# Performance work log

Measured on AMD Instinct MI355X. Metric: run time of the kernel, lower is better.

The kernel has to match this reference:

```python
import jax, jax.numpy as jnp
import numpy as np

B, S, D_MODEL, N_HEADS, MAX_LEN = 2, 1024, 1024, 16, 1024
D_K = D_MODEL // N_HEADS


def setup_inputs() -> dict:
    key = jax.random.key(0)
    ks = jax.random.split(key, 8)
    w_std = 1.0 / np.sqrt(D_MODEL)  # ~ torch Linear default scale
    inp = {
        "query": jax.random.normal(ks[0], (B, S, D_MODEL), jnp.float32),
        "key": jax.random.normal(ks[1], (B, S, D_MODEL), jnp.float32),
        "value": jax.random.normal(ks[2], (B, S, D_MODEL), jnp.float32),
        "Wq": jax.random.normal(ks[3], (D_MODEL, D_MODEL), jnp.float32) * w_std,
        "Wk": jax.random.normal(ks[4], (D_MODEL, D_MODEL), jnp.float32) * w_std,
        "Wv": jax.random.normal(ks[5], (D_MODEL, D_MODEL), jnp.float32) * w_std,
        "Wo": jax.random.normal(ks[6], (D_MODEL, D_MODEL), jnp.float32) * w_std,
        "bq": jnp.zeros((D_MODEL,), jnp.float32),
        "bk": jnp.zeros((D_MODEL,), jnp.float32),
        "bv": jnp.zeros((D_MODEL,), jnp.float32),
        "bo": jnp.zeros((D_MODEL,), jnp.float32),
        "Er": jax.random.normal(ks[7], (2 * MAX_LEN - 1, D_K), jnp.float32) * 0.02,
    }
    return inp


def _rel_positions(q_len, k_len, max_len):
    pos = jnp.arange(q_len)[:, None] - jnp.arange(k_len)[None, :]
    pos = jnp.clip(pos, -max_len + 1, max_len - 1)
    return pos + max_len - 1  # [q_len, k_len] indices into Er


def reference(query, key, value, Wq, Wk, Wv, Wo, bq, bk, bv, bo, Er):
    b, q_len, d_model = query.shape
    k_len = key.shape[1]
    d_k = Er.shape[-1]
    h = d_model // d_k
    scale = 1.0 / np.sqrt(d_k)

    def proj(x, W, bias):  # torch Linear: x @ W.T + b, then split heads -> [b,h,s,d_k]
        y = x @ W.T + bias
        return y.reshape(b, -1, h, d_k).transpose(0, 2, 1, 3)

    q = proj(query, Wq, bq)
    k = proj(key, Wk, bk)
    v = proj(value, Wv, bv)

    positions = _rel_positions(q_len, k_len, MAX_LEN)  # [q,k]
    # QEr[b,h,q,k] = sum_d q[b,h,q,d] * Er[positions[q,k], d]
    # computed as a full contraction against Er then a gather on the relative axis
    qe_all = jnp.einsum('bhqd,rd->bhqr', q, Er)  # [b,h,q,2*max_len-1]
    qer = jnp.take_along_axis(qe_all, positions[None, None, :, :], axis=-1)  # [b,h,q,k]

    qk = jnp.einsum('bhqd,bhkd->bhqk', q, k)
    scores = (qk + qer) * scale
    p_attn = jax.nn.softmax(scores, axis=-1)  # dropout=0.0 (eval)
    out = jnp.einsum('bhqk,bhkd->bhqd', p_attn, v)

    out = out.transpose(0, 2, 1, 3).reshape(b, q_len, h * d_k)
    return out @ Wo.T + bo
```

## Files before the change

kernel.cpp:

```cpp
#include <hip/hip_runtime.h>
#include <hip/hip_bf16.h>
#include <cstdint>
#include <cstddef>

typedef __attribute__((ext_vector_type(8))) short bf16x8;
typedef __attribute__((ext_vector_type(4))) float f32x4;
typedef unsigned short u16;
typedef unsigned int u32;

#define DEV static __device__ __forceinline__

constexpr int Sc = 1024, DMc = 1024, Hc = 16, DKc = 64;

DEV u16 f2bf(float f) {
  u32 u = __float_as_uint(f);
  return (u16)((u + 0x7FFFu + ((u >> 16) & 1u)) >> 16);
}
DEV float bf2f(u16 h) { return __uint_as_float(((u32)h) << 16); }

DEV u32 cvtpk(float a, float b) {
  u32 r;
  asm("v_cvt_pk_bf16_f32 %0, %1, %2" : "=v"(r) : "v"(a), "v"(b));
  return r;
}

#define GLDS16(g, l)                                                        \
  __builtin_amdgcn_global_load_lds(                                         \
      (const __attribute__((address_space(1))) void*)(g),                   \
      (__attribute__((address_space(3))) void*)(l), 16, 0, 0)

struct CvtJob { const float* in; u16* out; int rsh; int nreal; };
struct CvtArgs { CvtJob j[8]; int cum[8]; };

__global__ __launch_bounds__(256) void cvt_kernel(CvtArgs a) {
  int g = (int)(blockIdx.x * 256 + threadIdx.x);
  int jb = 0, base = 0;
  #pragma unroll
  for (int k = 0; k < 7; ++k) {
    bool m = g >= a.cum[k];
    jb += m ? 1 : 0;
    base = m ? a.cum[k] : base;
  }
  CvtJob job = a.j[jb];
  int ci = g - base;
  bf16x8 o = {};
  if (ci < job.nreal) {
    const float* src = job.in + (size_t)ci * 8;
    float4 v0 = *(const float4*)src;
    float4 v1 = *(const float4*)(src + 4);
    o[0] = (short)f2bf(v0.x); o[1] = (short)f2bf(v0.y);
    o[2] = (short)f2bf(v0.z); o[3] = (short)f2bf(v0.w);
    o[4] = (short)f2bf(v1.x); o[5] = (short)f2bf(v1.y);
    o[6] = (short)f2bf(v1.z); o[7] = (short)f2bf(v1.w);
  }
  int row = ci >> job.rsh;
  int co = (ci & ~7) | ((ci & 7) ^ (row & 7));
  *(bf16x8*)(job.out + (size_t)co * 8) = o;
}

struct GemmJob { const u16* A; const u16* W; const float* bias; void* out; const float* aux; };
struct GemmArgs { GemmJob p[3]; };

template<int BM, int BN, int MODE>
__global__ __launch_bounds__(256, 2) void gemm_bt(GemmArgs G) {
  constexpr int MI = BM / 32, NI = BN / 32;
  __shared__ __align__(16) u16 sA[2][BM * 64];
  __shared__ __align__(16) u16 sB[2][BN * 64];
  const int tid = threadIdx.x, lane = tid & 63, w = tid >> 6;
  const int cl = lane & 15, rg = lane >> 4;
  const int srow = lane >> 3, schk = lane & 7;
  int z, m0, n0;
  if (MODE == 0) {
    int id = blockIdx.x;
    if (id < 512) {
      z = id >> 8;
      int r = id & 255, xcd = r & 7, t = r >> 3;
      m0 = (xcd * 4 + (t & 3)) * 64;
      n0 = (t >> 2) * 128;
    } else {
      z = 2;
      int r = id - 512, xcd = r & 7, t = r >> 3;
      n0 = (xcd * 2 + (t & 1)) * 128;
      m0 = (t >> 1) * 64;
    }
  } else {
    z = 0;
    int id = blockIdx.x, xcd = id & 7, t = id >> 3;
    m0 = (xcd * 4 + (t & 3)) * 64;
    n0 = (t >> 2) * 64;
  }
  GemmJob P = G.p[z];
  constexpr int K = 1024;
  const int wm = (w >> 1) * (BM / 2), wn = (w & 1) * (BN / 2);
  f32x4 acc[MI][NI] = {};

  bf16x8 ma[2][2];
  float  ml[2][2];

  auto stage = [&](int kt, int b) {
    if (MODE == 0) {
      const u16* Ab = P.A + (size_t)m0 * K + kt * 64;
      #pragma unroll
      for (int i = 0; i < BM / 32; ++i)
        GLDS16(Ab + (size_t)(i * 32 + w * 8 + srow) * K + schk * 8, &sA[b][(i * 32 + w * 8) * 64]);
    } else {
      #pragma unroll
      for (int i = 0; i < 2; ++i) {
        int ch = i * 256 + tid, row = ch >> 3, c = ch & 7;
        int rgl = m0 + row, bb = rgl >> 10, s = rgl & 1023;
        const u16* o0 = P.A + ((size_t)(bb * 16 + kt) * 1024 + s) * 64 + c * 8;
        ma[i][0] = *(const bf16x8*)o0;
        ma[i][1] = *(const bf16x8*)(o0 + (size_t)32 * 1024 * 64);
        ml[i][0] = P.aux[(size_t)(bb * 16 + kt) * 1024 + s];
        ml[i][1] = P.aux[(size_t)(32 + bb * 16 + kt) * 1024 + s];
      }
    }
    const u16* Wb = P.W + (size_t)n0 * K + kt * 64;
    #pragma unroll
    for (int i = 0; i < BN / 32; ++i)
      GLDS16(Wb + (size_t)(i * 32 + w * 8 + srow) * K + schk * 8, &sB[b][(i * 32 + w * 8) * 64]);
  };

  auto commit = [&](int b) {
    #pragma unroll
    for (int i = 0; i < 2; ++i) {
      int ch = i * 256 + tid, row = ch >> 3, c = ch & 7;
      float rinv = 1.0f / (ml[i][0] + ml[i][1]);
      u32 pk[4];
      #pragma unroll
      for (int p = 0; p < 4; ++p) {
        float v0 = (bf2f((u16)ma[i][0][2 * p])     + bf2f((u16)ma[i][1][2 * p]))     * rinv;
        float v1 = (bf2f((u16)ma[i][0][2 * p + 1]) + bf2f((u16)ma[i][1][2 * p + 1])) * rinv;
        pk[p] = cvtpk(v0, v1);
      }
      bf16x8 v8;
      #pragma unroll
      for (int p = 0; p < 4; ++p) {
        v8[2 * p]     = (short)(pk[p] & 0xFFFF);
        v8[2 * p + 1] = (short)(pk[p] >> 16);
      }
      *(bf16x8*)(sA[b] + row * 64 + (c ^ (row & 7)) * 8) = v8;
    }
  };

  stage(0, 0);
  if (MODE == 1) commit(0);
  for (int kt = 0; kt < 16; ++kt) {
    __syncthreads();
    const int b = kt & 1;
    if (kt < 15) stage(kt + 1, b ^ 1);
    const u16* A_ = sA[b];
    const u16* B_ = sB[b];
    #pragma unroll
    for (int kk = 0; kk < 2; ++kk) {
      bf16x8 af[MI], bfr[NI];
      #pragma unroll
      for (int mi = 0; mi < MI; ++mi) {
        int row = wm + mi * 16 + cl;
        af[mi] = *(const bf16x8*)(A_ + row * 64 + ((kk * 4 + rg) ^ (row & 7)) * 8);
      }
      #pragma unroll
      for (int ni = 0; ni < NI; ++ni) {
        int row = wn + ni * 16 + cl;
        bfr[ni] = *(const bf16x8*)(B_ + row * 64 + ((kk * 4 + rg) ^ (row & 7)) * 8);
      }
      #pragma unroll
      for (int mi = 0; mi < MI; ++mi)
        #pragma unroll
        for (int ni = 0; ni < NI; ++ni)
          acc[mi][ni] = __builtin_amdgcn_mfma_f32_16x16x32_bf16(af[mi], bfr[ni], acc[mi][ni], 0, 0, 0);
    }
    if (MODE == 1 && kt < 15) commit(b ^ 1);
  }
  #pragma unroll
  for (int mi = 0; mi < MI; ++mi) {
    #pragma unroll
    for (int ni = 0; ni < NI; ++ni) {
      #pragma unroll
      for (int j = 0; j < 4; ++j) {
        int m = m0 + wm + mi * 16 + rg * 4 + j;
        int n = n0 + wn + ni * 16 + cl;
        if (MODE == 1) {
          ((float*)P.out)[(size_t)m * DMc + n] = acc[mi][ni][j] + P.bias[n];
        } else if (z < 2) {
          float v = acc[mi][ni][j] + P.bias[n];
          int h = n >> 6, d = n & 63;
          int c2 = (d >> 3) ^ (m & 7);
          ((u16*)P.out)[((size_t)((m >> 10) * Hc + h) * Sc + (m & 1023)) * DKc + c2 * 8 + (d & 7)] = f2bf(v);
        } else {
          float v = acc[mi][ni][j] + P.bias[m];
          int d = m & 63, h = m >> 6, bb = n >> 10, s = n & 1023;
          int c2 = ((s & 63) >> 3) ^ (d & 7);
          ((u16*)P.out)[((size_t)(bb * Hc + h) * DKc + d) * Sc + (s & ~63) + c2 * 8 + (s & 7)] = f2bf(v);
        }
      }
    }
  }
}

__global__ __launch_bounds__(256, 4) void attn_rel(
    const u16* __restrict__ qg, const u16* __restrict__ kg,
    const u16* __restrict__ vtg, const u16* __restrict__ erg,
    u16* __restrict__ Opart, float* __restrict__ lpart) {
  __shared__ __align__(16) u16 sK[64 * 64];
  __shared__ __align__(16) u16 sV[64 * 64];
  __shared__ __align__(16) u16 sU[4][1440];
  const int tid = threadIdx.x, lane = tid & 63, w = tid >> 6;
  const int cl = lane & 15, rg = lane >> 4;
  const int key = cl & 7;
  const int bh = blockIdx.x & 31, qt = (blockIdx.x >> 5) & 15, half = blockIdx.x >> 9;
  const int q0 = qt * 64, t0 = half * 8;

  const u16* qrow = qg + ((size_t)bh * Sc + q0 + w * 16 + cl) * DKc;
  bf16x8 qf0 = *(const bf16x8*)(qrow + (rg ^ key) * 8);
  bf16x8 qf1 = *(const bf16x8*)(qrow + ((rg + 4) ^ key) * 8);
  f32x4 oacc[4] = {};
  float lsum = 0.f;
  u16* Uw = sU[w];
  const u16* kbase = kg + (size_t)bh * Sc * DKc;
  const u16* vbase = vtg + (size_t)bh * DKc * Sc;

  auto stage = [&](int t) {
    const u16* ks = kbase + t * 64 * 64;
    #pragma unroll
    for (int i = 0; i < 2; ++i) {
      GLDS16(ks + (i * 32 + w * 8) * 64 + lane * 8, &sK[(i * 32 + w * 8) * 64]);
      GLDS16(vbase + (size_t)(i * 32 + w * 8 + (lane >> 3)) * Sc + t * 64 + (lane & 7) * 8,
             &sV[(i * 32 + w * 8) * 64]);
    }
  };

  stage(t0);
  for (int tt = 0; tt < 8; ++tt) {
    const int t = t0 + tt;
    __syncthreads();

    f32x4 sct[4];
    __builtin_amdgcn_s_setprio(1);
    #pragma unroll
    for (int nc = 0; nc < 4; ++nc) {
      const u16* kr = sK + (nc * 16 + cl) * 64;
      bf16x8 b0 = *(const bf16x8*)(kr + (rg ^ key) * 8);
      bf16x8 b1 = *(const bf16x8*)(kr + ((rg + 4) ^ key) * 8);
      f32x4 a = {};
      a = __builtin_amdgcn_mfma_f32_16x16x32_bf16(b0, qf0, a, 0, 0, 0);
      a = __builtin_amdgcn_mfma_f32_16x16x32_bf16(b1, qf1, a, 0, 0, 0);
      sct[nc] = a;
    }
    __builtin_amdgcn_s_setprio(0);
    const u16* ebase = erg + (size_t)(q0 + w * 16 - t * 64 + 960) * DKc;
    #pragma unroll
    for (int rc0 = 0; rc0 < 5; ++rc0) {
      const u16* er = ebase + (size_t)(rc0 * 16 + cl) * DKc;
      bf16x8 e0 = *(const bf16x8*)(er + (rg ^ key) * 8);
      bf16x8 e1 = *(const bf16x8*)(er + ((rg + 4) ^ key) * 8);
      f32x4 a = {};
      a = __builtin_amdgcn_mfma_f32_16x16x32_bf16(qf0, e0, a, 0, 0, 0);
      a = __builtin_amdgcn_mfma_f32_16x16x32_bf16(qf1, e1, a, 0, 0, 0);
      u16* tp = Uw + (rc0 * 16 + cl) * 18 + rg * 4;
      ushort2 lo, hi;
      lo.x = f2bf(a[0]); lo.y = f2bf(a[1]);
      hi.x = f2bf(a[2]); hi.y = f2bf(a[3]);
      *(ushort2*)tp = lo;
      *(ushort2*)(tp + 2) = hi;
    }
    __builtin_amdgcn_sched_barrier(0);
    float pv[4][4];
    #pragma unroll
    for (int nc = 0; nc < 4; ++nc) {
      #pragma unroll
      for (int j = 0; j < 4; ++j) {
        int r = cl + 63 - (nc * 16 + rg * 4 + j);
        float tval = bf2f(Uw[r * 18 + cl]);
        float p = __expf((sct[nc][j] + tval) * 0.125f);
        lsum += p;
        pv[nc][j] = p;
      }
    }
    __builtin_amdgcn_sched_barrier(0);
    #pragma unroll
    for (int nc = 0; nc < 4; ++nc) {
      uint2 pk2;
      pk2.x = cvtpk(pv[nc][0], pv[nc][1]);
      pk2.y = cvtpk(pv[nc][2], pv[nc][3]);
      *(ushort4*)(Uw + cl * 76 + nc * 16 + rg * 4) = __builtin_bit_cast(ushort4, pk2);
    }
    __builtin_amdgcn_sched_barrier(0);
    bf16x8 pa0 = *(const bf16x8*)(Uw + cl * 76 + rg * 8);
    bf16x8 pa1 = *(const bf16x8*)(Uw + cl * 76 + 32 + rg * 8);
    __builtin_amdgcn_s_setprio(1);
    #pragma unroll
    for (int dc = 0; dc < 4; ++dc) {
      const u16* vr = sV + (dc * 16 + cl) * 64;
      bf16x8 b0 = *(const bf16x8*)(vr + (rg ^ key) * 8);
      bf16x8 b1 = *(const bf16x8*)(vr + ((rg + 4) ^ key) * 8);
      oacc[dc] = __builtin_amdgcn_mfma_f32_16x16x32_bf16(pa0, b0, oacc[dc], 0, 0, 0);
      oacc[dc] = __builtin_amdgcn_mfma_f32_16x16x32_bf16(pa1, b1, oacc[dc], 0, 0, 0);
    }
    __builtin_amdgcn_s_setprio(0);
    __syncthreads();
    if (tt < 7) stage(t + 1);
  }
  lsum += __shfl_xor(lsum, 16);
  lsum += __shfl_xor(lsum, 32);
  const size_t pb = (size_t)(half * 32 + bh) * Sc;
  if (rg == 0) lpart[pb + q0 + w * 16 + cl] = lsum;
  u16* Ob = Opart + (pb + q0 + w * 16) * DKc;
  #pragma unroll
  for (int dc = 0; dc < 4; ++dc)
    #pragma unroll
    for (int j = 0; j < 4; ++j)
      Ob[(rg * 4 + j) * DKc + dc * 16 + cl] = f2bf(oacc[dc][j]);
}

extern "C" void kernel_launch(void* const* d_in, const int* in_sizes, int n_in,
                              void* d_out, int out_size, void* d_ws, size_t ws_size,
                              hipStream_t stream) {
  (void)in_sizes; (void)n_in; (void)out_size; (void)ws_size;
  const float* query = (const float*)d_in[0];
  const float* key_  = (const float*)d_in[1];
  const float* value = (const float*)d_in[2];
  const float* Wq = (const float*)d_in[3];
  const float* Wk = (const float*)d_in[4];
  const float* Wv = (const float*)d_in[5];
  const float* Wo = (const float*)d_in[6];
  const float* bq = (const float*)d_in[7];
  const float* bk = (const float*)d_in[8];
  const float* bv = (const float*)d_in[9];
  const float* bo = (const float*)d_in[10];
  const float* Er = (const float*)d_in[11];

  char* p = (char*)d_ws;
  size_t off = 0;
  auto alloc = [&](size_t bytes) {
    char* r = p + off;
    off += (bytes + 255) & ~(size_t)255;
    return r;
  };
  u16* Xq  = (u16*)alloc((size_t)2048 * 1024 * 2);
  u16* Xk  = (u16*)alloc((size_t)2048 * 1024 * 2);
  u16* Xv  = (u16*)alloc((size_t)2048 * 1024 * 2);
  u16* Wqb = (u16*)alloc((size_t)1024 * 1024 * 2);
  u16* Wkb = (u16*)alloc((size_t)1024 * 1024 * 2);
  u16* Wvb = (u16*)alloc((size_t)1024 * 1024 * 2);
  u16* Wob = (u16*)alloc((size_t)1024 * 1024 * 2);
  u16* Erb = (u16*)alloc((size_t)2048 * 64 * 2);
  u16* qh  = (u16*)alloc((size_t)2048 * 1024 * 2);
  u16* kh  = (u16*)alloc((size_t)2048 * 1024 * 2);
  u16* vt  = (u16*)alloc((size_t)2048 * 1024 * 2);
  u16* Opart = (u16*)alloc((size_t)2 * 32 * 1024 * 64 * 2);
  float* lpart = (float*)alloc((size_t)2 * 32 * 1024 * 4);

  CvtArgs ca;
  ca.j[0] = {query, Xq, 7, 262144};
  ca.j[1] = {key_,  Xk, 7, 262144};
  ca.j[2] = {value, Xv, 7, 262144};
  ca.j[3] = {Wq, Wqb, 7, 131072};
  ca.j[4] = {Wk, Wkb, 7, 131072};
  ca.j[5] = {Wv, Wvb, 7, 131072};
  ca.j[6] = {Wo, Wob, 7, 131072};
  ca.j[7] = {Er, Erb, 3, 16376};
  ca.cum[0] = 262144;  ca.cum[1] = 524288;  ca.cum[2] = 786432;
  ca.cum[3] = 917504;  ca.cum[4] = 1048576; ca.cum[5] = 1179648;
  ca.cum[6] = 1310720; ca.cum[7] = 1327104;
  cvt_kernel<<<dim3(5184, 1, 1), 256, 0, stream>>>(ca);

  GemmArgs gp;
  gp.p[0] = {Xq, Wqb, bq, (void*)qh, nullptr};
  gp.p[1] = {Xk, Wkb, bk, (void*)kh, nullptr};
  gp.p[2] = {Wvb, Xv, bv, (void*)vt, nullptr};
  gemm_bt<64, 128, 0><<<dim3(768, 1, 1), 256, 0, stream>>>(gp);

  attn_rel<<<dim3(1024, 1, 1), 256, 0, stream>>>(qh, kh, vt, Erb, Opart, lpart);

  GemmArgs go;
  go.p[0] = {Opart, Wob, bo, d_out, lpart};
  go.p[1] = go.p[0];
  go.p[2] = go.p[0];
  gemm_bt<64, 64, 1><<<dim3(512, 1, 1), 256, 0, stream>>>(go);
}
```

Measured before the change: 90.35 us.

## Split attention keys into four partitions and fold softmax scale into Q projection

The attention kernel now splits the key range into four quarters instead of two, doubling the grid to 2048 blocks, each processing four key tiles. The output-projection GEMM's A-loader sums four bf16 partial outputs and four partial row sums before normalising. The 1/sqrt(d_k) scale is applied in the Q projection epilogue, which removes a multiply per score in the attention inner loop. The trade-off is more partial-result traffic and larger workspace in exchange for more parallelism. Scaling Q before rounding to bf16 also slightly changes numerics.

```diff
diff --git a/kernel.cpp b/kernel.cpp
--- a/kernel.cpp
+++ b/kernel.cpp
@@ -58,7 +58,7 @@
   *(bf16x8*)(job.out + (size_t)co * 8) = o;
 }
 
-struct GemmJob { const u16* A; const u16* W; const float* bias; void* out; const float* aux; };
+struct GemmJob { const u16* A; const u16* W; const float* bias; void* out; const float* aux; float oscale; };
 struct GemmArgs { GemmJob p[3]; };
 
 template<int BM, int BN, int MODE>
@@ -94,8 +94,8 @@
   const int wm = (w >> 1) * (BM / 2), wn = (w & 1) * (BN / 2);
   f32x4 acc[MI][NI] = {};
 
-  bf16x8 ma[2][2];
-  float  ml[2][2];
+  bf16x8 ma[2][4];
+  float  ml[2][4];
 
   auto stage = [&](int kt, int b) {
     if (MODE == 0) {
@@ -109,10 +109,11 @@
         int ch = i * 256 + tid, row = ch >> 3, c = ch & 7;
         int rgl = m0 + row, bb = rgl >> 10, s = rgl & 1023;
         const u16* o0 = P.A + ((size_t)(bb * 16 + kt) * 1024 + s) * 64 + c * 8;
-        ma[i][0] = *(const bf16x8*)o0;
-        ma[i][1] = *(const bf16x8*)(o0 + (size_t)32 * 1024 * 64);
-        ml[i][0] = P.aux[(size_t)(bb * 16 + kt) * 1024 + s];
-        ml[i][1] = P.aux[(size_t)(32 + bb * 16 + kt) * 1024 + s];
+        #pragma unroll
+        for (int qq = 0; qq < 4; ++qq) {
+          ma[i][qq] = *(const bf16x8*)(o0 + (size_t)qq * 32 * 1024 * 64);
+          ml[i][qq] = P.aux[(size_t)(qq * 32 + bb * 16 + kt) * 1024 + s];
+        }
       }
     }
     const u16* Wb = P.W + (size_t)n0 * K + kt * 64;
@@ -125,12 +126,14 @@
     #pragma unroll
     for (int i = 0; i < 2; ++i) {
       int ch = i * 256 + tid, row = ch >> 3, c = ch & 7;
-      float rinv = 1.0f / (ml[i][0] + ml[i][1]);
+      float rinv = 1.0f / (ml[i][0] + ml[i][1] + ml[i][2] + ml[i][3]);
       u32 pk[4];
       #pragma unroll
       for (int p = 0; p < 4; ++p) {
-        float v0 = (bf2f((u16)ma[i][0][2 * p])     + bf2f((u16)ma[i][1][2 * p]))     * rinv;
-        float v1 = (bf2f((u16)ma[i][0][2 * p + 1]) + bf2f((u16)ma[i][1][2 * p + 1])) * rinv;
+        float v0 = (bf2f((u16)ma[i][0][2 * p])     + bf2f((u16)ma[i][1][2 * p]) +
+                    bf2f((u16)ma[i][2][2 * p])     + bf2f((u16)ma[i][3][2 * p]))     * rinv;
+        float v1 = (bf2f((u16)ma[i][0][2 * p + 1]) + bf2f((u16)ma[i][1][2 * p + 1]) +
+                    bf2f((u16)ma[i][2][2 * p + 1]) + bf2f((u16)ma[i][3][2 * p + 1])) * rinv;
         pk[p] = cvtpk(v0, v1);
       }
       bf16x8 v8;
@@ -183,7 +186,7 @@
         if (MODE == 1) {
           ((float*)P.out)[(size_t)m * DMc + n] = acc[mi][ni][j] + P.bias[n];
         } else if (z < 2) {
-          float v = acc[mi][ni][j] + P.bias[n];
+          float v = (acc[mi][ni][j] + P.bias[n]) * P.oscale;
           int h = n >> 6, d = n & 63;
           int c2 = (d >> 3) ^ (m & 7);
           ((u16*)P.out)[((size_t)((m >> 10) * Hc + h) * Sc + (m & 1023)) * DKc + c2 * 8 + (d & 7)] = f2bf(v);
@@ -208,8 +211,8 @@
   const int tid = threadIdx.x, lane = tid & 63, w = tid >> 6;
   const int cl = lane & 15, rg = lane >> 4;
   const int key = cl & 7;
-  const int bh = blockIdx.x & 31, qt = (blockIdx.x >> 5) & 15, half = blockIdx.x >> 9;
-  const int q0 = qt * 64, t0 = half * 8;
+  const int bh = blockIdx.x & 31, qt = (blockIdx.x >> 5) & 15, quarter = blockIdx.x >> 9;
+  const int q0 = qt * 64, t0 = quarter * 4;
 
   const u16* qrow = qg + ((size_t)bh * Sc + q0 + w * 16 + cl) * DKc;
   bf16x8 qf0 = *(const bf16x8*)(qrow + (rg ^ key) * 8);
@@ -231,7 +234,7 @@
   };
 
   stage(t0);
-  for (int tt = 0; tt < 8; ++tt) {
+  for (int tt = 0; tt < 4; ++tt) {
     const int t = t0 + tt;
     __syncthreads();
 
@@ -272,7 +275,7 @@
       for (int j = 0; j < 4; ++j) {
         int r = cl + 63 - (nc * 16 + rg * 4 + j);
         float tval = bf2f(Uw[r * 18 + cl]);
-        float p = __expf((sct[nc][j] + tval) * 0.125f);
+        float p = __expf(sct[nc][j] + tval);
         lsum += p;
         pv[nc][j] = p;
       }
@@ -299,11 +302,11 @@
     }
     __builtin_amdgcn_s_setprio(0);
     __syncthreads();
-    if (tt < 7) stage(t + 1);
+    if (tt < 3) stage(t + 1);
   }
   lsum += __shfl_xor(lsum, 16);
   lsum += __shfl_xor(lsum, 32);
-  const size_t pb = (size_t)(half * 32 + bh) * Sc;
+  const size_t pb = (size_t)(quarter * 32 + bh) * Sc;
   if (rg == 0) lpart[pb + q0 + w * 16 + cl] = lsum;
   u16* Ob = Opart + (pb + q0 + w * 16) * DKc;
   #pragma unroll
@@ -348,8 +351,8 @@
   u16* qh  = (u16*)alloc((size_t)2048 * 1024 * 2);
   u16* kh  = (u16*)alloc((size_t)2048 * 1024 * 2);
   u16* vt  = (u16*)alloc((size_t)2048 * 1024 * 2);
-  u16* Opart = (u16*)alloc((size_t)2 * 32 * 1024 * 64 * 2);
-  float* lpart = (float*)alloc((size_t)2 * 32 * 1024 * 4);
+  u16* Opart = (u16*)alloc((size_t)4 * 32 * 1024 * 64 * 2);
+  float* lpart = (float*)alloc((size_t)4 * 32 * 1024 * 4);
 
   CvtArgs ca;
   ca.j[0] = {query, Xq, 7, 262144};
@@ -366,15 +369,15 @@
   cvt_kernel<<<dim3(5184, 1, 1), 256, 0, stream>>>(ca);
 
   GemmArgs gp;
-  gp.p[0] = {Xq, Wqb, bq, (void*)qh, nullptr};
-  gp.p[1] = {Xk, Wkb, bk, (void*)kh, nullptr};
-  gp.p[2] = {Wvb, Xv, bv, (void*)vt, nullptr};
+  gp.p[0] = {Xq, Wqb, bq, (void*)qh, nullptr, 0.125f};
+  gp.p[1] = {Xk, Wkb, bk, (void*)kh, nullptr, 1.0f};
+  gp.p[2] = {Wvb, Xv, bv, (void*)vt, nullptr, 1.0f};
   gemm_bt<64, 128, 0><<<dim3(768, 1, 1), 256, 0, stream>>>(gp);
 
-  attn_rel<<<dim3(1024, 1, 1), 256, 0, stream>>>(qh, kh, vt, Erb, Opart, lpart);
+  attn_rel<<<dim3(2048, 1, 1), 256, 0, stream>>>(qh, kh, vt, Erb, Opart, lpart);
 
   GemmArgs go;
-  go.p[0] = {Opart, Wob, bo, d_out, lpart};
+  go.p[0] = {Opart, Wob, bo, d_out, lpart, 1.0f};
   go.p[1] = go.p[0];
   go.p[2] = go.p[0];
   gemm_bt<64, 64, 1><<<dim3(512, 1, 1), 256, 0, stream>>>(go);
```

After: 97.90 us. 8.4% more time.
